# Kernel tuning notes

Hardware: AMD Instinct MI355X
Metric: run time of the kernel (lower is better)

## Reference

```python
import jax, jax.numpy as jnp
import numpy as np

B, D, L = 8, 512, 4096
NHEAD = 8
HEAD_DIM = D // NHEAD
TRUNC_STD = 0.02


def setup_inputs() -> dict:
    key = jax.random.key(0)
    ks = jax.random.split(key, 7)
    return {
        "x": jax.random.normal(ks[0], (B, D, L, 1), jnp.float32),
        "y": jax.random.normal(ks[1], (B, D, 1, 1), jnp.float32),
        "Wq": jax.random.normal(ks[2], (D, D), jnp.float32) * TRUNC_STD,
        "Wk": jax.random.normal(ks[3], (D, D), jnp.float32) * TRUNC_STD,
        "Wv": jax.random.normal(ks[4], (D, D), jnp.float32) * TRUNC_STD,
        "WO_ring": jax.random.normal(ks[5], (D, D), jnp.float32) * TRUNC_STD,
        "bO_ring": jnp.zeros((D,), jnp.float32),
        "WO_star": jax.random.normal(ks[6], (D, D), jnp.float32) * TRUNC_STD,
        "bO_star": jnp.zeros((D,), jnp.float32),
    }


def reference(x, y, Wq, Wk, Wv, WO_ring, bO_ring, WO_star, bO_star):
    Bx, Dx, Lx, _ = x.shape
    hd = Dx // NHEAD
    scale = 1.0 / np.sqrt(hd).astype(np.float32)

    # concat relay token on the sequence axis, project q/k/v over channels
    xy = jnp.concatenate([x, y], axis=2)[..., 0]            # [B, D, L+1]
    xy = jnp.transpose(xy, (0, 2, 1))                       # [B, L+1, D]
    q = jnp.transpose(xy @ Wq, (0, 2, 1))                   # [B, D, L+1]
    k = jnp.transpose(xy @ Wk, (0, 2, 1))
    v = jnp.transpose(xy @ Wv, (0, 2, 1))

    # ---- ring (local window-3 + relay) attention over the L node tokens ----
    qn = q[:, :, :Lx].reshape(Bx, NHEAD, hd, Lx)            # [B,n,h,L]
    kn, vn = k[:, :, :Lx], v[:, :, :Lx]                     # [B,D,L]
    kr, vr = k[:, :, Lx], v[:, :, Lx]                       # [B,D]

    def window3(t):
        # extract_patches SAME with size 3: slot w holds t[:, :, l-1+w], zero-padded
        tp = jnp.pad(t, ((0, 0), (0, 0), (1, 1)))
        tw = jnp.stack([tp[:, :, w:w + Lx] for w in range(3)], axis=2)  # [B,D,3,L]
        return tw.reshape(Bx, NHEAD, hd, 3, Lx)

    kr_b = jnp.broadcast_to(kr.reshape(Bx, NHEAD, hd, 1, 1), (Bx, NHEAD, hd, 1, Lx))
    vr_b = jnp.broadcast_to(vr.reshape(Bx, NHEAD, hd, 1, 1), (Bx, NHEAD, hd, 1, Lx))
    kw = jnp.concatenate([window3(kn), kr_b], axis=3)       # [B,n,h,4,L]
    vw = jnp.concatenate([window3(vn), vr_b], axis=3)

    scores = jnp.einsum('bnhl,bnhwl->bnwl', qn, kw) * scale  # [B,n,4,L]
    alphas = jax.nn.softmax(scores, axis=2)                  # softmax over window
    att = jnp.einsum('bnwl,bnhwl->bnhl', alphas, vw).reshape(Bx, Dx, Lx)
    nodes = jnp.einsum('bdl,de->bel', att, WO_ring) + bO_ring[None, :, None]
    nodes = nodes[..., None]                                 # [B, D, L, 1]

    # ---- star (relay) attention: relay query attends to all L+1 tokens ----
    qr = q[:, :, Lx].reshape(Bx, NHEAD, 1, hd)              # [B,n,1,h]
    ka = k.reshape(Bx, NHEAD, hd, Lx + 1)                   # [B,n,h,L+1]
    va = v.reshape(Bx, NHEAD, hd, Lx + 1)
    s = jnp.einsum('bnoh,bnhl->bnol', qr, ka) * scale       # [B,n,1,L+1]
    a = jax.nn.softmax(s, axis=-1)
    att_r = jnp.einsum('bnol,bnhl->bnoh', a, va).reshape(Bx, Dx)
    relay = (att_r @ WO_star + bO_star).reshape(Bx, Dx, 1, 1)

    return nodes, relay
```

## Files before the change

kernel.cpp:

```cpp
#include <hip/hip_runtime.h>

#define BB 8
#define DD 512
#define LL 4096
#define NH 8
#define HD 64
#define SCALE 0.125f
#define NCH 16
#define CH 256

typedef __attribute__((ext_vector_type(8))) short short8;
typedef __attribute__((ext_vector_type(4))) float f32x4;

static __device__ __forceinline__ float bf2f(unsigned short u) {
  union { float f; unsigned int i; } c; c.i = ((unsigned int)u) << 16; return c.f;
}
static __device__ __forceinline__ unsigned short f2bf(float f) {
  union { float f; unsigned int i; } c; c.f = f;
  unsigned int i = c.i;
  unsigned int r = (i + 0x7fffu + ((i >> 16) & 1u)) >> 16;
  return (unsigned short)r;
}

static __device__ __forceinline__ void gload_lds16(const void* g, void* l) {
  __builtin_amdgcn_global_load_lds(
      (const __attribute__((address_space(1))) void*)g,
      (__attribute__((address_space(3))) void*)l, 16, 0, 0);
}

static __device__ __forceinline__ float waveSum(float v) {
#pragma unroll
  for (int o = 32; o; o >>= 1) v += __shfl_down(v, o, 64);
  return v;
}
static __device__ __forceinline__ float waveMax(float v) {
#pragma unroll
  for (int o = 32; o; o >>= 1) v = fmaxf(v, __shfl_down(v, o, 64));
  return v;
}
static __device__ __forceinline__ float grp8Sum(float v) {
  v += __shfl_xor(v, 1, 8);
  v += __shfl_xor(v, 2, 8);
  v += __shfl_xor(v, 4, 8);
  return v;
}
static __device__ float blockSum(float v, float* red) {
  const int lane = threadIdx.x & 63, wid = threadIdx.x >> 6;
  const int nw = (int)(blockDim.x >> 6);
  v = waveSum(v);
  if (lane == 0) red[wid] = v;
  __syncthreads();
  if (wid == 0) {
    float t = (lane < nw) ? red[lane] : 0.f;
    t = waveSum(t);
    if (lane == 0) red[0] = t;
  }
  __syncthreads();
  float r = red[0];
  __syncthreads();
  return r;
}
static __device__ float blockMax(float v, float* red) {
  const int lane = threadIdx.x & 63, wid = threadIdx.x >> 6;
  const int nw = (int)(blockDim.x >> 6);
  v = waveMax(v);
  if (lane == 0) red[wid] = v;
  __syncthreads();
  if (wid == 0) {
    float t = (lane < nw) ? red[lane] : -1e30f;
    t = waveMax(t);
    if (lane == 0) red[0] = t;
  }
  __syncthreads();
  float r = red[0];
  __syncthreads();
  return r;
}

__global__ __launch_bounds__(256) void prep_w(
    const float* __restrict__ win, unsigned short* __restrict__ wout) {
  const int d0 = blockIdx.y * 64;
  const int m0 = blockIdx.x * 64;
  __shared__ float t[64][65];
  const int tid = threadIdx.x;
  const int r = tid >> 4;
  const int c4 = (tid & 15) * 4;
#pragma unroll
  for (int p = 0; p < 4; p++) {
    const float4 v = *(const float4*)(win + (size_t)(d0 + p * 16 + r) * DD + m0 + c4);
    *(float4*)&t[p * 16 + r][c4] = v;
  }
  __syncthreads();
#pragma unroll
  for (int p = 0; p < 4; p++) {
    const int ll = p * 16 + r;
    ushort4 o;
    o.x = f2bf(t[c4 + 0][ll]);
    o.y = f2bf(t[c4 + 1][ll]);
    o.z = f2bf(t[c4 + 2][ll]);
    o.w = f2bf(t[c4 + 3][ll]);
    *(ushort4*)(wout + (size_t)(m0 + ll) * DD + d0 + c4) = o;
  }
}

__global__ __launch_bounds__(256) void prep_x(
    const float* __restrict__ x, unsigned short* __restrict__ xt) {
  const int b = blockIdx.z;
  const int e0 = blockIdx.y * 64;
  const int l0 = blockIdx.x * 64;
  __shared__ float t[64][65];
  const int tid = threadIdx.x;
  const int r = tid >> 4;
  const int c4 = (tid & 15) * 4;
  const float* xb = x + (size_t)b * DD * LL;
#pragma unroll
  for (int p = 0; p < 4; p++) {
    const float4 v = *(const float4*)(xb + (size_t)(e0 + p * 16 + r) * LL + l0 + c4);
    *(float4*)&t[p * 16 + r][c4] = v;
  }
  __syncthreads();
#pragma unroll
  for (int p = 0; p < 4; p++) {
    const int ll = p * 16 + r;
    ushort4 o;
    o.x = f2bf(t[c4 + 0][ll]);
    o.y = f2bf(t[c4 + 1][ll]);
    o.z = f2bf(t[c4 + 2][ll]);
    o.w = f2bf(t[c4 + 3][ll]);
    *(ushort4*)(xt + ((size_t)b * LL + l0 + ll) * DD + e0 + c4) = o;
  }
}

#define STAGEH(g, s)                                       \
  do {                                                     \
    gload_lds16((g) + sgoff, (s) + sloff);                 \
    gload_lds16((g) + sgoff + 32, (s) + sloff + 4096);     \
  } while (0)

#define READ_A(dst, base, ib)                                           \
  _Pragma("unroll") for (int i = 0; i < 4; i++) {                       \
    dst[i][0] = *(const short8*)((base) + ((ib) + i) * 512);            \
    dst[i][1] = *(const short8*)((base) + ((ib) + i) * 512 + 4096);     \
  }

#define READ_B(base, qn_)                                               \
  _Pragma("unroll") for (int j = 0; j < 2; j++) {                       \
    bb[j][0] = *(const short8*)((base) + (qn_) * 1024 + j * 512);       \
    bb[j][1] = *(const short8*)((base) + (qn_) * 1024 + j * 512 + 4096);\
  }

#define MFMA16(AF, IO, JO)                                                    \
  __builtin_amdgcn_s_setprio(1);                                              \
  _Pragma("unroll") for (int i = 0; i < 4; i++)                               \
  _Pragma("unroll") for (int j = 0; j < 2; j++) {                             \
    acc[(IO) + i][(JO) + j] = __builtin_amdgcn_mfma_f32_16x16x32_bf16(        \
        AF[i][0], bb[j][0], acc[(IO) + i][(JO) + j], 0, 0, 0);                \
    acc[(IO) + i][(JO) + j] = __builtin_amdgcn_mfma_f32_16x16x32_bf16(        \
        AF[i][1], bb[j][1], acc[(IO) + i][(JO) + j], 0, 0, 0);                \
  }                                                                           \
  __builtin_amdgcn_s_setprio(0);

#define PHASE_SYNC_PRE                                     \
  __builtin_amdgcn_s_barrier();                            \
  asm volatile("s_waitcnt lgkmcnt(0)" ::: "memory");       \
  __builtin_amdgcn_sched_barrier(0);

#define PHASE_SYNC_POST                                    \
  __builtin_amdgcn_sched_barrier(0);                       \
  __builtin_amdgcn_s_barrier();

__global__ __launch_bounds__(512, 2) void qkv_mfma_8ph(
    const unsigned short* __restrict__ Wt, const unsigned short* __restrict__ Xt,
    unsigned short* __restrict__ qn, unsigned short* __restrict__ kn,
    unsigned short* __restrict__ vn) {
  extern __shared__ __align__(16) unsigned short sm[];
  const int b = blockIdx.z;
  const int m0 = blockIdx.y * 256;
  const int n0 = blockIdx.x * 256;
  const int tid = threadIdx.x;
  const int lane = tid & 63, w = tid >> 6;
  const int wm = w >> 2, wn = w & 3;
  const int l15 = lane & 15, lh = lane >> 4;

  const unsigned short* Ag = Wt + (size_t)m0 * DD;
  const unsigned short* Bg = Xt + ((size_t)b * LL + n0) * DD;

  const int kswz = (lh << 3) ^ ((l15 & 8) << 1);
  const unsigned short* aB = sm + wm * 8192 + l15 * 32 + kswz;
  const unsigned short* bB = sm + 32768 + (wn >> 1) * 8192 + (wn & 1) * 2048 +
                             l15 * 32 + kswz;

  const int srow = (w << 4) + (lane >> 2);
  const size_t sgoff = (size_t)srow * DD + ((size_t)(((lane & 3) << 3) ^ ((srow & 8) << 1)));
  const int sloff = w * 512;

  f32x4 acc[8][4];
#pragma unroll
  for (int i = 0; i < 8; i++)
#pragma unroll
    for (int j = 0; j < 4; j++) acc[i][j] = (f32x4){0.f, 0.f, 0.f, 0.f};

  STAGEH(Ag, sm);
  STAGEH(Ag + 128 * DD, sm + 8192);
  STAGEH(Bg, sm + 32768);
  STAGEH(Bg + 128 * DD, sm + 32768 + 8192);
  STAGEH(Ag + 64, sm + 16384);
  STAGEH(Ag + 128 * DD + 64, sm + 16384 + 8192);
  asm volatile("s_waitcnt vmcnt(4)" ::: "memory");
  __builtin_amdgcn_s_barrier();

  short8 a0[4][2], a1[4][2], bb[2][2];
  for (int u = 0; u < 8; ++u) {
    const int slot = u & 1;
    const unsigned short* aS = aB + slot * 16384;
    const unsigned short* bS = bB + slot * 16384;
    const unsigned short* An = Ag + (u + 2) * 64;
    const unsigned short* Bn = Bg + (u + 1) * 64;
    unsigned short* sAd = sm + slot * 16384;
    unsigned short* sBd = sm + 32768 + (slot ^ 1) * 16384;

    READ_A(a0, aS, 0);
    READ_B(bS, 0);
    if (u < 7) STAGEH(Bn, sBd);
    PHASE_SYNC_PRE
    MFMA16(a0, 0, 0)
    PHASE_SYNC_POST
    READ_A(a1, aS, 4);
    if (u < 7) STAGEH(Bn + 128 * DD, sBd + 8192);
    PHASE_SYNC_PRE
    MFMA16(a1, 4, 0)
    PHASE_SYNC_POST
    READ_B(bS, 1);
    if (u < 6) STAGEH(An, sAd);
    PHASE_SYNC_PRE
    MFMA16(a0, 0, 2)
    PHASE_SYNC_POST
    if (u < 6) STAGEH(An + 128 * DD, sAd + 8192);
    __builtin_amdgcn_s_barrier();
    asm volatile("s_waitcnt lgkmcnt(0)" ::: "memory");
    __builtin_amdgcn_sched_barrier(0);
    MFMA16(a1, 4, 2)
    __builtin_amdgcn_sched_barrier(0);
    if (u < 6) {
      asm volatile("s_waitcnt vmcnt(4)" ::: "memory");
    } else if (u == 6) {
      asm volatile("s_waitcnt vmcnt(0)" ::: "memory");
    }
    __builtin_amdgcn_s_barrier();
  }

  __syncthreads();
#pragma unroll
  for (int i = 0; i < 8; i++)
#pragma unroll
    for (int j = 0; j < 4; j++) {
      const int dloc = wm * 128 + i * 16 + lh * 4;
      const int lloc = wn * 64 + j * 16 + l15;
      ushort4 pk;
      pk.x = f2bf(acc[i][j][0]);
      pk.y = f2bf(acc[i][j][1]);
      pk.z = f2bf(acc[i][j][2]);
      pk.w = f2bf(acc[i][j][3]);
      *(ushort4*)((char*)sm + ((lloc * 512 + dloc * 2) ^ ((lloc & 7) << 4))) = pk;
    }
  __syncthreads();
  const int sector = m0 >> 9;
  unsigned short* outp = ((sector == 0) ? qn : (sector == 1) ? kn : vn) +
                         (size_t)b * LL * DD + (m0 & 511);
#pragma unroll
  for (int it = 0; it < 16; it++) {
    const int flat = it * 8192 + tid * 16;
    const int lloc = flat >> 9;
    const int off = flat & 511;
    const short8 vdat =
        *(const short8*)((const char*)sm + lloc * 512 + (off ^ ((lloc & 7) << 4)));
    *(short8*)(outp + (size_t)(n0 + lloc) * DD + (off >> 1)) = vdat;
  }
}

__global__ __launch_bounds__(256) void nodes_mfma(
    const unsigned short* __restrict__ Wt, const unsigned short* __restrict__ At,
    const float* __restrict__ bo, float* __restrict__ out) {
  const int b = blockIdx.z;
  const int m0 = blockIdx.y * 128;
  const int n0 = blockIdx.x * 128;
  __shared__ short As[128 * 32];
  __shared__ short Bs[128 * 32];
  const int tid = threadIdx.x;
  const int lane = tid & 63, w = tid >> 6;
  const int wm = w & 1, wn = w >> 1;

  const unsigned short* Ag = Wt + (size_t)m0 * DD;
  const unsigned short* Bg = At + ((size_t)b * LL + n0) * DD;
  const int srow = lane >> 2;
  const int scol = (lane & 3) * 8;

  f32x4 acc[4][4];
#pragma unroll
  for (int i = 0; i < 4; i++)
#pragma unroll
    for (int j = 0; j < 4; j++) acc[i][j] = (f32x4){0.f, 0.f, 0.f, 0.f};

  for (int k0 = 0; k0 < DD; k0 += 32) {
    __syncthreads();
#pragma unroll
    for (int p = 0; p < 2; p++) {
      const int c = w * 2 + p;
      gload_lds16(Ag + (size_t)(c * 16 + srow) * DD + k0 + scol, (short*)As + c * 16 * 32);
      gload_lds16(Bg + (size_t)(c * 16 + srow) * DD + k0 + scol, (short*)Bs + c * 16 * 32);
    }
    __syncthreads();
    short8 af[4], bfr[4];
#pragma unroll
    for (int i = 0; i < 4; i++)
      af[i] = *(const short8*)&As[(wm * 64 + i * 16 + (lane & 15)) * 32 + (lane >> 4) * 8];
#pragma unroll
    for (int j = 0; j < 4; j++)
      bfr[j] = *(const short8*)&Bs[(wn * 64 + j * 16 + (lane & 15)) * 32 + (lane >> 4) * 8];
#pragma unroll
    for (int i = 0; i < 4; i++)
#pragma unroll
      for (int j = 0; j < 4; j++)
        acc[i][j] = __builtin_amdgcn_mfma_f32_16x16x32_bf16(af[i], bfr[j], acc[i][j], 0, 0, 0);
  }

  float* outp = out + (size_t)b * DD * LL;
  const int ebase = m0 + wm * 64;
  const int col0 = n0 + wn * 64 + (lane & 15);
#pragma unroll
  for (int i = 0; i < 4; i++) {
    const int e0 = ebase + i * 16 + (lane >> 4) * 4;
#pragma unroll
    for (int j = 0; j < 4; j++) {
      const int cc = col0 + j * 16;
#pragma unroll
      for (int r = 0; r < 4; r++)
        outp[(size_t)(e0 + r) * LL + cc] = acc[i][j][r] + bo[e0 + r];
    }
  }
}

__global__ __launch_bounds__(256) void relay_qkv(
    const float* __restrict__ y, const float* __restrict__ Wq,
    const float* __restrict__ Wk, const float* __restrict__ Wv,
    float* __restrict__ qr, float* __restrict__ kr, float* __restrict__ vr) {
  const int b = blockIdx.y;
  const int d = blockIdx.x * 256 + threadIdx.x;
  __shared__ float ys[DD];
  for (int i = threadIdx.x; i < DD; i += 256) ys[i] = y[b * DD + i];
  __syncthreads();
  float aq = 0.f, ak = 0.f, av = 0.f;
  for (int e = 0; e < DD; e++) {
    const float yv = ys[e];
    aq = fmaf(yv, Wq[(size_t)e * DD + d], aq);
    ak = fmaf(yv, Wk[(size_t)e * DD + d], ak);
    av = fmaf(yv, Wv[(size_t)e * DD + d], av);
  }
  qr[b * DD + d] = aq;
  kr[b * DD + d] = ak;
  vr[b * DD + d] = av;
}

__global__ __launch_bounds__(256) void local_attn(
    const unsigned short* __restrict__ qn, const unsigned short* __restrict__ kn,
    const unsigned short* __restrict__ vn, const float* __restrict__ kr,
    const float* __restrict__ vr, unsigned short* __restrict__ att_t) {
  const int b = blockIdx.z, n = blockIdx.y;
  const int tid = threadIdx.x;
  const int li = tid >> 3, dl = tid & 7;
  const int l = blockIdx.x * 32 + li;
  __shared__ float krs[HD], vrs[HD];
  const int rb = b * DD + n * HD;
  if (tid < HD) { krs[tid] = kr[rb + tid]; vrs[tid] = vr[rb + tid]; }
  __syncthreads();

  const size_t rowbase = ((size_t)b * LL + l) * DD + n * HD + dl * 8;
  const unsigned short* qp = qn + rowbase;
  const unsigned short* kp = kn + rowbase;
  const unsigned short* vp = vn + rowbase;
  const bool has_m = (l > 0), has_p = (l < LL - 1);
  const long moff = has_m ? -(long)DD : 0;
  const long poff = has_p ? (long)DD : 0;

  const short8 q8 = *(const short8*)qp;
  const short8 km8 = *(const short8*)(kp + moff);
  const short8 k08 = *(const short8*)kp;
  const short8 kp8 = *(const short8*)(kp + poff);

  float s0 = 0.f, s1 = 0.f, s2 = 0.f, s3 = 0.f;
  float qf[8];
#pragma unroll
  for (int j = 0; j < 8; j++) {
    qf[j] = bf2f((unsigned short)q8[j]);
    s0 = fmaf(qf[j], bf2f((unsigned short)km8[j]), s0);
    s1 = fmaf(qf[j], bf2f((unsigned short)k08[j]), s1);
    s2 = fmaf(qf[j], bf2f((unsigned short)kp8[j]), s2);
    s3 = fmaf(qf[j], krs[dl * 8 + j], s3);
  }
  s0 = grp8Sum(s0) * SCALE;
  s1 = grp8Sum(s1) * SCALE;
  s2 = grp8Sum(s2) * SCALE;
  s3 = grp8Sum(s3) * SCALE;
  if (!has_m) s0 = 0.f;
  if (!has_p) s2 = 0.f;
  const float m = fmaxf(fmaxf(s0, s1), fmaxf(s2, s3));
  const float e0 = __expf(s0 - m), e1 = __expf(s1 - m);
  const float e2 = __expf(s2 - m), e3 = __expf(s3 - m);
  const float inv = 1.f / (e0 + e1 + e2 + e3);
  const float a0 = has_m ? e0 * inv : 0.f;
  const float a1 = e1 * inv;
  const float a2 = has_p ? e2 * inv : 0.f;
  const float a3 = e3 * inv;

  const short8 vm8 = *(const short8*)(vp + moff);
  const short8 v08 = *(const short8*)vp;
  const short8 vp8 = *(const short8*)(vp + poff);
  short8 o8;
#pragma unroll
  for (int j = 0; j < 8; j++) {
    float o = a0 * bf2f((unsigned short)vm8[j]) + a1 * bf2f((unsigned short)v08[j]) +
              a2 * bf2f((unsigned short)vp8[j]) + a3 * vrs[dl * 8 + j];
    o8[j] = (short)f2bf(o);
  }
  *(short8*)(att_t + rowbase) = o8;
}

__global__ __launch_bounds__(256) void relay_attn_part(
    const float* __restrict__ qr, const unsigned short* __restrict__ kn,
    const unsigned short* __restrict__ vn, float* __restrict__ part) {
  const int ch = blockIdx.x, n = blockIdx.y, b = blockIdx.z;
  const int tid = threadIdx.x;
  const int li = tid >> 3, dl = tid & 7;
  __shared__ float qs[HD];
  __shared__ float sv[CH];
  __shared__ float red[17];
  __shared__ float os[32][68];
  const int rb = b * DD + n * HD;
  if (tid < HD) qs[tid] = qr[rb + tid];
  __syncthreads();
  const size_t base = ((size_t)b * LL + ch * CH) * DD + n * HD + dl * 8;

#pragma unroll
  for (int it = 0; it < 8; it++) {
    const int lr2 = it * 32 + li;
    const short8 kc = *(const short8*)(kn + base + (size_t)lr2 * DD);
    float p = 0.f;
#pragma unroll
    for (int j = 0; j < 8; j++) p = fmaf(qs[dl * 8 + j], bf2f((unsigned short)kc[j]), p);
    p = grp8Sum(p);
    if (dl == 0) sv[lr2] = p * SCALE;
  }
  __syncthreads();
  const float s = sv[tid];
  const float m = blockMax(s, red);
  const float pp = __expf(s - m);
  sv[tid] = pp;
  const float sum = blockSum(pp, red);

  float oc[8];
#pragma unroll
  for (int j = 0; j < 8; j++) oc[j] = 0.f;
#pragma unroll
  for (int it = 0; it < 8; it++) {
    const int lr2 = it * 32 + li;
    const float p = sv[lr2];
    const short8 vc = *(const short8*)(vn + base + (size_t)lr2 * DD);
#pragma unroll
    for (int j = 0; j < 8; j++) oc[j] = fmaf(p, bf2f((unsigned short)vc[j]), oc[j]);
  }
#pragma unroll
  for (int j = 0; j < 8; j++) os[li][dl * 8 + j] = oc[j];
  __syncthreads();
  float* po = part + (((size_t)b * NH + n) * NCH + ch) * 68;
  if (tid < HD) {
    float t = 0.f;
#pragma unroll 8
    for (int g = 0; g < 32; g++) t += os[g][tid];
    po[tid] = t;
  }
  if (tid == 64) { po[64] = m; po[65] = sum; }
}

__global__ __launch_bounds__(64) void relay_attn_combine(
    const float* __restrict__ qr, const float* __restrict__ krr,
    const float* __restrict__ vrr, const float* __restrict__ part,
    float* __restrict__ attr) {
  const int n = blockIdx.x, b = blockIdx.y;
  const int h = threadIdx.x;
  const int rb = b * DD + n * HD;
  float t = qr[rb + h] * krr[rb + h];
  t = waveSum(t);
  const float s_r = __shfl(t, 0, 64) * SCALE;
  const float* po = part + (((size_t)b * NH + n) * NCH) * 68;
  float M = s_r;
#pragma unroll
  for (int c = 0; c < NCH; c++) M = fmaxf(M, po[c * 68 + 64]);
  float S = __expf(s_r - M);
  float o = S * vrr[rb + h];
#pragma unroll
  for (int c = 0; c < NCH; c++) {
    const float e = __expf(po[c * 68 + 64] - M);
    S = fmaf(po[c * 68 + 65], e, S);
    o = fmaf(po[c * 68 + h], e, o);
  }
  attr[rb + h] = o / S;
}

__global__ __launch_bounds__(256) void relay_proj(
    const float* __restrict__ attr, const float* __restrict__ Wstar,
    const float* __restrict__ bstar, float* __restrict__ out) {
  const int b = blockIdx.y;
  const int e = blockIdx.x * 256 + threadIdx.x;
  __shared__ float as[DD];
  for (int i = threadIdx.x; i < DD; i += 256) as[i] = attr[b * DD + i];
  __syncthreads();
  float acc = bstar[e];
  for (int d = 0; d < DD; d++) acc = fmaf(as[d], Wstar[(size_t)d * DD + e], acc);
  out[(size_t)BB * DD * LL + b * DD + e] = acc;
}

extern "C" void kernel_launch(void* const* d_in, const int* in_sizes, int n_in,
                              void* d_out, int out_size, void* d_ws, size_t ws_size,
                              hipStream_t stream) {
  const float* x   = (const float*)d_in[0];
  const float* y   = (const float*)d_in[1];
  const float* Wq  = (const float*)d_in[2];
  const float* Wk  = (const float*)d_in[3];
  const float* Wv  = (const float*)d_in[4];
  const float* WOr = (const float*)d_in[5];
  const float* bOr = (const float*)d_in[6];
  const float* WOs = (const float*)d_in[7];
  const float* bOs = (const float*)d_in[8];
  float* out = (float*)d_out;

  char* ws = (char*)d_ws;
  const size_t SZ = (size_t)BB * DD * LL * sizeof(unsigned short);
  unsigned short* qn  = (unsigned short*)(ws);
  unsigned short* kn  = (unsigned short*)(ws + SZ);
  unsigned short* vn  = (unsigned short*)(ws + 2 * SZ);
  unsigned short* xt  = (unsigned short*)(ws + 3 * SZ);
  unsigned short* att_t = xt;
  unsigned short* Wallt = (unsigned short*)(ws + 4 * SZ);
  unsigned short* WOrt  = (unsigned short*)(ws + 4 * SZ + 1536 * 512 * 2);
  float* qr   = (float*)(ws + 4 * SZ + 2048 * 512 * 2);
  float* kr   = qr + BB * DD;
  float* vr   = kr + BB * DD;
  float* attr = vr + BB * DD;
  float* part = attr + BB * DD;

  static int smaxset = 0;
  if (!smaxset) {
    (void)hipFuncSetAttribute((const void*)qkv_mfma_8ph,
                              hipFuncAttributeMaxDynamicSharedMemorySize, 131072);
    smaxset = 1;
  }

  prep_w<<<dim3(8, 8), 256, 0, stream>>>(Wq, Wallt);
  prep_w<<<dim3(8, 8), 256, 0, stream>>>(Wk, Wallt + (size_t)512 * 512);
  prep_w<<<dim3(8, 8), 256, 0, stream>>>(Wv, Wallt + (size_t)1024 * 512);
  prep_w<<<dim3(8, 8), 256, 0, stream>>>(WOr, WOrt);
  prep_x<<<dim3(64, 8, BB), 256, 0, stream>>>(x, xt);

  qkv_mfma_8ph<<<dim3(16, 6, BB), 512, 131072, stream>>>(Wallt, xt, qn, kn, vn);
  relay_qkv<<<dim3(DD / 256, BB), 256, 0, stream>>>(y, Wq, Wk, Wv, qr, kr, vr);
  local_attn<<<dim3(LL / 32, NH, BB), 256, 0, stream>>>(qn, kn, vn, kr, vr, att_t);
  nodes_mfma<<<dim3(32, 4, BB), 256, 0, stream>>>(WOrt, att_t, bOr, out);
  relay_attn_part<<<dim3(NCH, NH, BB), 256, 0, stream>>>(qr, kn, vn, part);
  relay_attn_combine<<<dim3(NH, BB), 64, 0, stream>>>(qr, kr, vr, part, attr);
  relay_proj<<<dim3(DD / 256, BB), 256, 0, stream>>>(attr, WOs, bOs, out);
}
```

Baseline: 316.0 us.

## Merge weight prep launches and deepen B prefetch in QKV GEMM pipeline

Four separate weight transpose/convert launches are folded into one launch that picks its source and destination from the z grid index, removing launch overhead. In the QKV MFMA kernel, the B operand is now prefetched two k-steps ahead like A, with both halves staged after the second phase and the vmcnt wait raised from 4 to 8 outstanding loads. The aim is more latency hiding for global-to-LDS loads, at the cost of reordered staging and tighter correctness dependence on the slot/wait bookkeeping.

```diff
diff --git a/kernel.cpp b/kernel.cpp
--- a/kernel.cpp
+++ b/kernel.cpp
@@ -77,8 +77,14 @@
   return r;
 }
 
-__global__ __launch_bounds__(256) void prep_w(
-    const float* __restrict__ win, unsigned short* __restrict__ wout) {
+__global__ __launch_bounds__(256) void prep_w4(
+    const float* __restrict__ w0, const float* __restrict__ w1,
+    const float* __restrict__ w2, const float* __restrict__ w3,
+    unsigned short* __restrict__ o0, unsigned short* __restrict__ o1,
+    unsigned short* __restrict__ o2, unsigned short* __restrict__ o3) {
+  const int s = blockIdx.z;
+  const float* win = (s == 0) ? w0 : (s == 1) ? w1 : (s == 2) ? w2 : w3;
+  unsigned short* wout = (s == 0) ? o0 : (s == 1) ? o1 : (s == 2) ? o2 : o3;
   const int d0 = blockIdx.y * 64;
   const int m0 = blockIdx.x * 64;
   __shared__ float t[64][65];
@@ -206,7 +212,9 @@
   STAGEH(Bg + 128 * DD, sm + 32768 + 8192);
   STAGEH(Ag + 64, sm + 16384);
   STAGEH(Ag + 128 * DD + 64, sm + 16384 + 8192);
-  asm volatile("s_waitcnt vmcnt(4)" ::: "memory");
+  STAGEH(Bg + 64, sm + 32768 + 16384);
+  STAGEH(Bg + 128 * DD + 64, sm + 32768 + 16384 + 8192);
+  asm volatile("s_waitcnt vmcnt(8)" ::: "memory");
   __builtin_amdgcn_s_barrier();
 
   short8 a0[4][2], a1[4][2], bb[2][2];
@@ -215,34 +223,38 @@
     const unsigned short* aS = aB + slot * 16384;
     const unsigned short* bS = bB + slot * 16384;
     const unsigned short* An = Ag + (u + 2) * 64;
-    const unsigned short* Bn = Bg + (u + 1) * 64;
+    const unsigned short* Bn = Bg + (u + 2) * 64;
     unsigned short* sAd = sm + slot * 16384;
-    unsigned short* sBd = sm + 32768 + (slot ^ 1) * 16384;
+    unsigned short* sBd = sm + 32768 + slot * 16384;
 
     READ_A(a0, aS, 0);
     READ_B(bS, 0);
-    if (u < 7) STAGEH(Bn, sBd);
     PHASE_SYNC_PRE
     MFMA16(a0, 0, 0)
     PHASE_SYNC_POST
     READ_A(a1, aS, 4);
-    if (u < 7) STAGEH(Bn + 128 * DD, sBd + 8192);
     PHASE_SYNC_PRE
     MFMA16(a1, 4, 0)
     PHASE_SYNC_POST
     READ_B(bS, 1);
-    if (u < 6) STAGEH(An, sAd);
+    if (u < 6) {
+      STAGEH(An, sAd);
+      STAGEH(An + 128 * DD, sAd + 8192);
+    }
     PHASE_SYNC_PRE
     MFMA16(a0, 0, 2)
     PHASE_SYNC_POST
-    if (u < 6) STAGEH(An + 128 * DD, sAd + 8192);
+    if (u < 6) {
+      STAGEH(Bn, sBd);
+      STAGEH(Bn + 128 * DD, sBd + 8192);
+    }
     __builtin_amdgcn_s_barrier();
     asm volatile("s_waitcnt lgkmcnt(0)" ::: "memory");
     __builtin_amdgcn_sched_barrier(0);
     MFMA16(a1, 4, 2)
     __builtin_amdgcn_sched_barrier(0);
     if (u < 6) {
-      asm volatile("s_waitcnt vmcnt(4)" ::: "memory");
+      asm volatile("s_waitcnt vmcnt(8)" ::: "memory");
     } else if (u == 6) {
       asm volatile("s_waitcnt vmcnt(0)" ::: "memory");
     }
@@ -555,10 +567,9 @@
     smaxset = 1;
   }
 
-  prep_w<<<dim3(8, 8), 256, 0, stream>>>(Wq, Wallt);
-  prep_w<<<dim3(8, 8), 256, 0, stream>>>(Wk, Wallt + (size_t)512 * 512);
-  prep_w<<<dim3(8, 8), 256, 0, stream>>>(Wv, Wallt + (size_t)1024 * 512);
-  prep_w<<<dim3(8, 8), 256, 0, stream>>>(WOr, WOrt);
+  prep_w4<<<dim3(8, 8, 4), 256, 0, stream>>>(
+      Wq, Wk, Wv, WOr,
+      Wallt, Wallt + (size_t)512 * 512, Wallt + (size_t)1024 * 512, WOrt);
   prep_x<<<dim3(64, 8, BB), 256, 0, stream>>>(x, xt);
 
   qkv_mfma_8ph<<<dim3(16, 6, BB), 512, 131072, stream>>>(Wallt, xt, qn, kn, vn);
```

Measured after the change: 312.9 us. No clear change (-1.0%).

## Merge weight-prep launches and swizzle GEMM workgroup order for XCD locality

Applied to the files above, without the earlier changes.

Folds four separate weight transpose/convert launches into one launch indexed by blockIdx.z, removing three kernel launch overheads. It also remaps workgroup IDs in the QKV and output-projection GEMMs so that consecutive workgroups scheduled round-robin across the 8 XCDs share the same batch and neighbouring tiles. The aim is better L2 reuse of the X/attention and weight tiles per XCD. The remap assumes the hardware dispatches workgroups round-robin across 8 XCDs, and it adds a small amount of integer index arithmetic.

```diff
diff --git a/kernel.cpp b/kernel.cpp
--- a/kernel.cpp
+++ b/kernel.cpp
@@ -77,8 +77,14 @@
   return r;
 }
 
-__global__ __launch_bounds__(256) void prep_w(
-    const float* __restrict__ win, unsigned short* __restrict__ wout) {
+__global__ __launch_bounds__(256) void prep_w4(
+    const float* __restrict__ w0, const float* __restrict__ w1,
+    const float* __restrict__ w2, const float* __restrict__ w3,
+    unsigned short* __restrict__ o0, unsigned short* __restrict__ o1,
+    unsigned short* __restrict__ o2, unsigned short* __restrict__ o3) {
+  const int s = blockIdx.z;
+  const float* win = (s == 0) ? w0 : (s == 1) ? w1 : (s == 2) ? w2 : w3;
+  unsigned short* wout = (s == 0) ? o0 : (s == 1) ? o1 : (s == 2) ? o2 : o3;
   const int d0 = blockIdx.y * 64;
   const int m0 = blockIdx.x * 64;
   __shared__ float t[64][65];
@@ -174,9 +180,12 @@
     unsigned short* __restrict__ qn, unsigned short* __restrict__ kn,
     unsigned short* __restrict__ vn) {
   extern __shared__ __align__(16) unsigned short sm[];
-  const int b = blockIdx.z;
-  const int m0 = blockIdx.y * 256;
-  const int n0 = blockIdx.x * 256;
+  const int wgid = blockIdx.x + 16 * (blockIdx.y + 6 * blockIdx.z);
+  const int swz = (wgid & 7) * 96 + (wgid >> 3);
+  const int b = swz / 96;
+  const int rem = swz - b * 96;
+  const int n0 = (rem / 6) * 256;
+  const int m0 = (rem % 6) * 256;
   const int tid = threadIdx.x;
   const int lane = tid & 63, w = tid >> 6;
   const int wm = w >> 2, wn = w & 3;
@@ -281,9 +290,12 @@
 __global__ __launch_bounds__(256) void nodes_mfma(
     const unsigned short* __restrict__ Wt, const unsigned short* __restrict__ At,
     const float* __restrict__ bo, float* __restrict__ out) {
-  const int b = blockIdx.z;
-  const int m0 = blockIdx.y * 128;
-  const int n0 = blockIdx.x * 128;
+  const int wgid = blockIdx.x + 32 * (blockIdx.y + 4 * blockIdx.z);
+  const int swz = (wgid & 7) * 128 + (wgid >> 3);
+  const int b = swz >> 7;
+  const int rem = swz & 127;
+  const int n0 = (rem >> 2) * 128;
+  const int m0 = (rem & 3) * 128;
   __shared__ short As[128 * 32];
   __shared__ short Bs[128 * 32];
   const int tid = threadIdx.x;
@@ -555,10 +567,9 @@
     smaxset = 1;
   }
 
-  prep_w<<<dim3(8, 8), 256, 0, stream>>>(Wq, Wallt);
-  prep_w<<<dim3(8, 8), 256, 0, stream>>>(Wk, Wallt + (size_t)512 * 512);
-  prep_w<<<dim3(8, 8), 256, 0, stream>>>(Wv, Wallt + (size_t)1024 * 512);
-  prep_w<<<dim3(8, 8), 256, 0, stream>>>(WOr, WOrt);
+  prep_w4<<<dim3(8, 8, 4), 256, 0, stream>>>(
+      Wq, Wk, Wv, WOr,
+      Wallt, Wallt + (size_t)512 * 512, Wallt + (size_t)1024 * 512, WOrt);
   prep_x<<<dim3(64, 8, BB), 256, 0, stream>>>(x, xt);
 
   qkv_mfma_8ph<<<dim3(16, 6, BB), 512, 131072, stream>>>(Wallt, xt, qn, kn, vn);
```

Result: no change. 310.6 us (-1.7%).
